# Kernel optimization log

Hardware: AMD Instinct MI355X
Metric: run time of the kernel (lower is better)

## Reference

```python
import jax, jax.numpy as jnp
import numpy as np

# Winograd F(2x2, 3x3) transform matrices (standard Lavin & Gray form).
# The original torch module encodes B^T / A^T but applies them with elementwise
# mul (a bug that crashes); the intended math is Y = A^T [ (G g G^T) .* (B^T d B) ] A
# per 4x4 input tile with stride 2, which equals a valid 3x3 conv. We implement
# that intended Winograd computation faithfully and vectorized.
_BT = jnp.array([[1., 0., -1., 0.],
                 [0., 1., 1., 0.],
                 [0., -1., 1., 0.],
                 [0., 1., 0., -1.]], dtype=jnp.float32)
_G = jnp.array([[1., 0., 0.],
                [0.5, 0.5, 0.5],
                [0.5, -0.5, 0.5],
                [0., 0., 1.]], dtype=jnp.float32)
_AT = jnp.array([[1., 1., 1., 0.],
                 [0., 1., -1., -1.]], dtype=jnp.float32)


def setup_inputs() -> dict:
    key = jax.random.key(0)
    k1, k2 = jax.random.split(key)
    X = jax.random.normal(k1, (16, 32, 258, 258), dtype=jnp.float32)
    K = jax.random.normal(k2, (32, 32, 3, 3), dtype=jnp.float32)
    return {"X": X, "K": K}


def _winograd_conv(X, K):
    B_, C, H, W = X.shape
    Fo = K.shape[0]
    blocks = (H - 3) // 2 + 1  # number of 2x2 output tiles per spatial dim

    # Kernel transform: U = G K G^T  -> (Fo, C, 4, 4)
    U = jnp.einsum('ij,fcjk,lk->fcil', _G, K, _G)

    # Extract overlapping 4x4 tiles with stride 2: (B, C, blocks, blocks, 4, 4)
    i0 = jnp.arange(blocks) * 2
    win = i0[:, None] + jnp.arange(4)[None, :]          # (blocks, 4)
    tiles = X[:, :, win, :]                              # (B, C, blocks, 4, W)
    tiles = tiles[:, :, :, :, win]                       # (B, C, blocks, 4, blocks, 4)
    tiles = tiles.transpose(0, 1, 2, 4, 3, 5)            # (B, C, p, q, 4, 4)

    # Input transform: V = B^T d B
    V = jnp.einsum('ij,bcpqjk,lk->bcpqil', _BT, tiles, _BT)

    # Elementwise multiply in transform domain, summed over input channels
    M = jnp.einsum('fcil,bcpqil->bfpqil', U, V)          # (B, Fo, p, q, 4, 4)

    # Inverse transform: Y = A^T M A -> (B, Fo, p, q, 2, 2)
    Y = jnp.einsum('ij,bfpqjk,lk->bfpqil', _AT, M, _AT)

    # Stitch 2x2 tiles back: (B, Fo, 2*blocks, 2*blocks)
    out = Y.transpose(0, 1, 2, 4, 3, 5).reshape(B_, Fo, 2 * blocks, 2 * blocks)
    return out


def reference(X, K):
    return _winograd_conv(X, K)
```

## Files before the change

### kernel.cpp

```cpp
#include <hip/hip_runtime.h>
#include <stdint.h>

typedef __attribute__((ext_vector_type(8))) short bf16x8;
typedef __attribute__((ext_vector_type(4))) float f32x4;

__device__ inline float bflo(uint32_t w) { union { uint32_t i; float f; } v; v.i = w << 16; return v.f; }
__device__ inline float bfhi(uint32_t w) { union { uint32_t i; float f; } v; v.i = w & 0xffff0000u; return v.f; }
__device__ inline uint32_t f2bf(float f) { union { float f; uint32_t i; } v; v.f = f; return (v.i + 0x8000u) >> 16; }
__device__ inline uint32_t pk(float lo, float hi) { return f2bf(lo) | (f2bf(hi) << 16); }

__global__ __launch_bounds__(256) void wg_filter(const float* __restrict__ Kk, uint32_t* __restrict__ Ud)
{
    const int idx = blockIdx.x * 256 + threadIdx.x;
    if (idx >= 512) return;
    const int cp = idx & 15, f = idx >> 4;
    float u[2][16];
    #pragma unroll
    for (int h = 0; h < 2; h++) {
        const float* kp = Kk + (f * 32 + cp * 2 + h) * 9;
        float k00 = kp[0], k01 = kp[1], k02 = kp[2];
        float k10 = kp[3], k11 = kp[4], k12 = kp[5];
        float k20 = kp[6], k21 = kp[7], k22 = kp[8];
        float t[4][3];
        t[0][0] = k00; t[0][1] = k01; t[0][2] = k02;
        t[1][0] = 0.5f * (k00 + k10 + k20); t[1][1] = 0.5f * (k01 + k11 + k21); t[1][2] = 0.5f * (k02 + k12 + k22);
        t[2][0] = 0.5f * (k00 - k10 + k20); t[2][1] = 0.5f * (k01 - k11 + k21); t[2][2] = 0.5f * (k02 - k12 + k22);
        t[3][0] = k20; t[3][1] = k21; t[3][2] = k22;
        #pragma unroll
        for (int i = 0; i < 4; i++) {
            float a0 = t[i][0], a1 = t[i][1], a2 = t[i][2];
            u[h][i * 4 + 0] = a0;
            u[h][i * 4 + 1] = 0.5f * (a0 + a1 + a2);
            u[h][i * 4 + 2] = 0.5f * (a0 - a1 + a2);
            u[h][i * 4 + 3] = a2;
        }
    }
    const int base = ((cp >> 2) * 32 + f) * 4 + (cp & 3);
    #pragma unroll
    for (int p = 0; p < 16; p++) Ud[p * 512 + base] = pk(u[0][p], u[1][p]);
}

__global__ __launch_bounds__(256, 5) void wg_main(
    const float* __restrict__ X, const uint16_t* __restrict__ U, float* __restrict__ out)
{
    __shared__ __align__(16) uint32_t Pl[2896];
    __shared__ __align__(16) uint16_t Vl[8192];

    const int tid = threadIdx.x;
    const int qb = blockIdx.x;
    const int pb = blockIdx.y;
    const int b  = blockIdx.z;
    const int y0 = pb * 8, x0 = qb * 16;

    for (int s = tid; s < 1440; s += 256) {
        const int pr = s / 90;
        const int r  = s - pr * 90;
        const int row = r / 9, seg = r - row * 9;
        const float* g0 = X + ((size_t)((b * 32 + pr * 2) * 258 + y0 + row)) * 258 + x0 + seg * 2;
        float2 a = *(const float2*)g0;
        float2 c = *(const float2*)(g0 + 258 * 258);
        const int pbase = pr * 181 + row * 18 + seg * 2;
        Pl[pbase]     = pk(a.x, c.x);
        Pl[pbase + 1] = pk(a.y, c.y);
    }
    __syncthreads();

    const int wave = tid >> 6, lane = tid & 63;
    const int fh = wave & 1, tb = wave >> 1;
    const int l15 = lane & 15, lq = lane >> 4;
    const uint16_t* Ub = U + (lq * 32 + fh * 16 + l15) * 8;
    const uint16_t* Vb = Vl + ((tb * 4 + lq) * 16 + l15) * 8;
    uint32_t* vp = (uint32_t*)Vl;

    float y[4][4];
    #pragma unroll
    for (int r = 0; r < 4; r++)
        #pragma unroll
        for (int j = 0; j < 4; j++) y[r][j] = 0.f;

    #pragma unroll
    for (int ch = 0; ch < 2; ch++) {
        #pragma unroll
        for (int it = 0; it < 2; it++) {
            const int rem  = it * 4 + wave;
            const int tblk = rem & 1, cpH = rem >> 1;
            const int cp2  = tid & 3, t15 = (tid >> 2) & 15;
            const int cp   = cpH * 4 + cp2;
            const int tt   = tblk * 16 + t15;
            const int tr   = tt >> 3, tc = tt & 7;
            const uint32_t* pp = &Pl[cp * 181 + (tr * 2 + ch) * 18 + tc * 2];
            float d0[3][4], d1[3][4];
            #pragma unroll
            for (int j = 0; j < 3; j++)
                #pragma unroll
                for (int k = 0; k < 4; k++) {
                    uint32_t w = pp[j * 18 + k];
                    d0[j][k] = bflo(w); d1[j][k] = bfhi(w);
                }
            float e00[4], e01[4], e10[4], e11[4];
            #pragma unroll
            for (int k = 0; k < 4; k++) {
                if (ch == 0) {
                    e00[k] = d0[0][k] - d0[2][k];  e10[k] = d1[0][k] - d1[2][k];
                    e01[k] = d0[1][k] + d0[2][k];  e11[k] = d1[1][k] + d1[2][k];
                } else {
                    e00[k] = d0[1][k] - d0[0][k];  e10[k] = d1[1][k] - d1[0][k];
                    e01[k] = d0[0][k] - d0[2][k];  e11[k] = d1[0][k] - d1[2][k];
                }
            }
            const int vbase = ((tblk * 4 + cpH) * 16 + t15) * 4 + cp2;
            #pragma unroll
            for (int row = 0; row < 2; row++) {
                const float* e0 = row ? e01 : e00;
                const float* e1 = row ? e11 : e10;
                vp[(row * 4 + 0) * 512 + vbase] = pk(e0[0] - e0[2], e1[0] - e1[2]);
                vp[(row * 4 + 1) * 512 + vbase] = pk(e0[1] + e0[2], e1[1] + e1[2]);
                vp[(row * 4 + 2) * 512 + vbase] = pk(e0[2] - e0[1], e1[2] - e1[1]);
                vp[(row * 4 + 3) * 512 + vbase] = pk(e0[1] - e0[3], e1[1] - e1[3]);
            }
        }
        __syncthreads();

        f32x4 acc[8];
        #pragma unroll
        for (int p8 = 0; p8 < 8; p8++) acc[p8] = (f32x4){0.f, 0.f, 0.f, 0.f};
        #pragma unroll
        for (int p8 = 0; p8 < 8; p8++) {
            bf16x8 a = *(const bf16x8*)(Ub + (ch * 8 + p8) * 1024);
            bf16x8 v = *(const bf16x8*)(Vb + p8 * 1024);
            acc[p8] = __builtin_amdgcn_mfma_f32_16x16x32_bf16(a, v, acc[p8], 0, 0, 0);
        }
        if (ch == 0) __syncthreads();

        #pragma unroll
        for (int r = 0; r < 4; r++) {
            #pragma unroll
            for (int ii = 0; ii < 2; ii++) {
                const int i = ch * 2 + ii;
                float m0 = acc[ii * 4 + 0][r], m1 = acc[ii * 4 + 1][r];
                float m2 = acc[ii * 4 + 2][r], m3 = acc[ii * 4 + 3][r];
                float c0 = m0 + m1 + m2, c1 = m1 - m2 - m3;
                if (i == 0)      { y[r][0] += c0; y[r][1] += c1; }
                else if (i == 1) { y[r][0] += c0; y[r][1] += c1; y[r][2] += c0; y[r][3] += c1; }
                else if (i == 2) { y[r][0] += c0; y[r][1] += c1; y[r][2] -= c0; y[r][3] -= c1; }
                else             { y[r][2] -= c0; y[r][3] -= c1; }
            }
        }
    }

    const int t = tb * 16 + l15;
    const int trr = t >> 3, tcc = t & 7;
    const int p = pb * 4 + trr, q = qb * 8 + tcc;
    #pragma unroll
    for (int r = 0; r < 4; r++) {
        const int f = fh * 16 + lq * 4 + r;
        float* op = out + ((size_t)(b * 32 + f) * 256 + 2 * p) * 256 + 2 * q;
        *(float2*)op = make_float2(y[r][0], y[r][1]);
        *(float2*)(op + 256) = make_float2(y[r][2], y[r][3]);
    }
}

__device__ inline uint16_t f2bf16_rne(float f) {
    union { float f; uint32_t i; } v; v.f = f;
    uint32_t x = v.i;
    uint32_t r = x + 0x7fffu + ((x >> 16) & 1u);
    return (uint16_t)(r >> 16);
}
__global__ __launch_bounds__(256) void winograd_fallback(
    const float* __restrict__ X, const float* __restrict__ K, float* __restrict__ out)
{
    __shared__ uint16_t Ul[16384];
    __shared__ uint16_t Vl[16384];
    __shared__ uint16_t Pl[32 * 242];
    const int tid = threadIdx.x;
    const int qb = blockIdx.x, pb = blockIdx.y, b = blockIdx.z;
    for (int idx = tid; idx < 1024; idx += 256) {
        const int f = idx >> 5, c = idx & 31;
        const float* kp = K + (f * 32 + c) * 9;
        float k00 = kp[0], k01 = kp[1], k02 = kp[2];
        float k10 = kp[3], k11 = kp[4], k12 = kp[5];
        float k20 = kp[6], k21 = kp[7], k22 = kp[8];
        float t[4][3];
        t[0][0] = k00; t[0][1] = k01; t[0][2] = k02;
        t[1][0] = 0.5f * (k00 + k10 + k20); t[1][1] = 0.5f * (k01 + k11 + k21); t[1][2] = 0.5f * (k02 + k12 + k22);
        t[2][0] = 0.5f * (k00 - k10 + k20); t[2][1] = 0.5f * (k01 - k11 + k21); t[2][2] = 0.5f * (k02 - k12 + k22);
        t[3][0] = k20; t[3][1] = k21; t[3][2] = k22;
        const int ubase = ((c >> 3) * 32 + f) * 8 + (c & 7);
        #pragma unroll
        for (int i = 0; i < 4; i++) {
            float a0 = t[i][0], a1 = t[i][1], a2 = t[i][2];
            Ul[(i * 4 + 0) * 1024 + ubase] = f2bf16_rne(a0);
            Ul[(i * 4 + 1) * 1024 + ubase] = f2bf16_rne(0.5f * (a0 + a1 + a2));
            Ul[(i * 4 + 2) * 1024 + ubase] = f2bf16_rne(0.5f * (a0 - a1 + a2));
            Ul[(i * 4 + 3) * 1024 + ubase] = f2bf16_rne(a2);
        }
    }
    const int y0 = pb * 8, x0 = qb * 16;
    for (int s = tid; s < 2880; s += 256) {
        const int c = s / 90;
        const int r = s % 90;
        const int row = r / 9, seg = r % 9;
        const float* gp = X + ((b * 32 + c) * 258 + (y0 + row)) * 258 + x0 + seg * 2;
        float2 g = *(const float2*)gp;
        uint32_t packed = (uint32_t)f2bf16_rne(g.x) | ((uint32_t)f2bf16_rne(g.y) << 16);
        *(uint32_t*)&Pl[c * 242 + row * 24 + seg * 2] = packed;
    }
    __syncthreads();
    for (int idx = tid; idx < 1024; idx += 256) {
        const int c = idx & 31, tt = idx >> 5;
        const int tr = tt >> 3, tc = tt & 7;
        const uint16_t* pp = &Pl[c * 242 + (tr * 2) * 24 + tc * 2];
        float d[4][4];
        #pragma unroll
        for (int j = 0; j < 4; j++) {
            uint32_t w0 = *(const uint32_t*)&pp[j * 24];
            uint32_t w1 = *(const uint32_t*)&pp[j * 24 + 2];
            d[j][0] = bflo(w0); d[j][1] = bfhi(w0);
            d[j][2] = bflo(w1); d[j][3] = bfhi(w1);
        }
        float bt[4][4];
        #pragma unroll
        for (int k = 0; k < 4; k++) {
            bt[0][k] = d[0][k] - d[2][k];
            bt[1][k] = d[1][k] + d[2][k];
            bt[2][k] = d[2][k] - d[1][k];
            bt[3][k] = d[1][k] - d[3][k];
        }
        const int vbase = (((tt >> 4) * 4 + (c >> 3)) * 16 + (tt & 15)) * 8 + (c & 7);
        #pragma unroll
        for (int i = 0; i < 4; i++) {
            float b0 = bt[i][0], b1 = bt[i][1], b2 = bt[i][2], b3 = bt[i][3];
            Vl[(i * 4 + 0) * 1024 + vbase] = f2bf16_rne(b0 - b2);
            Vl[(i * 4 + 1) * 1024 + vbase] = f2bf16_rne(b1 + b2);
            Vl[(i * 4 + 2) * 1024 + vbase] = f2bf16_rne(b2 - b1);
            Vl[(i * 4 + 3) * 1024 + vbase] = f2bf16_rne(b1 - b3);
        }
    }
    __syncthreads();
    const int wave = tid >> 6, lane = tid & 63;
    const int fh = wave & 1, tb = wave >> 1;
    const int l15 = lane & 15, lq = lane >> 4;
    f32x4 acc[16];
    #pragma unroll
    for (int p = 0; p < 16; p++) acc[p] = (f32x4){0.f, 0.f, 0.f, 0.f};
    #pragma unroll
    for (int p = 0; p < 16; p++) {
        bf16x8 a = *(const bf16x8*)&Ul[p * 1024 + (lq * 32 + fh * 16 + l15) * 8];
        bf16x8 bv = *(const bf16x8*)&Vl[p * 1024 + ((tb * 4 + lq) * 16 + l15) * 8];
        acc[p] = __builtin_amdgcn_mfma_f32_16x16x32_bf16(a, bv, acc[p], 0, 0, 0);
    }
    #pragma unroll
    for (int r = 0; r < 4; r++) {
        const int f = fh * 16 + lq * 4 + r;
        const int t = tb * 16 + l15;
        const int tr = t >> 3, tc = t & 7;
        const int p = pb * 4 + tr, q = qb * 8 + tc;
        float m[4][4];
        #pragma unroll
        for (int i = 0; i < 4; i++)
            #pragma unroll
            for (int l = 0; l < 4; l++)
                m[i][l] = acc[i * 4 + l][r];
        float s0[4], s1[4];
        #pragma unroll
        for (int k = 0; k < 4; k++) {
            s0[k] = m[0][k] + m[1][k] + m[2][k];
            s1[k] = m[1][k] - m[2][k] - m[3][k];
        }
        float* op = out + ((size_t)(b * 32 + f) * 256 + 2 * p) * 256 + 2 * q;
        *(float2*)op = make_float2(s0[0] + s0[1] + s0[2], s0[1] - s0[2] - s0[3]);
        *(float2*)(op + 256) = make_float2(s1[0] + s1[1] + s1[2], s1[1] - s1[2] - s1[3]);
    }
}

extern "C" void kernel_launch(void* const* d_in, const int* in_sizes, int n_in,
                              void* d_out, int out_size, void* d_ws, size_t ws_size,
                              hipStream_t stream) {
    const float* X = (const float*)d_in[0];
    const float* K = (const float*)d_in[1];
    float* out = (float*)d_out;
    dim3 grid(16, 32, 16);
    if (ws_size >= 32768) {
        wg_filter<<<2, 256, 0, stream>>>(K, (uint32_t*)d_ws);
        wg_main<<<grid, 256, 0, stream>>>(X, (const uint16_t*)d_ws, out);
    } else {
        winograd_fallback<<<grid, 256, 0, stream>>>(X, K, out);
    }
}
```

Measured before the change: 95.42 us.

## Use packed f32 math, hardware bf16 pack, vector LDS access, and early U loads

Replaces scalar float add/sub in the input transform with v_pk_add_f32 on paired channels. Manual bf16 rounding is replaced with v_cvt_pk_bf16_f32, which also changes the rounding behaviour. The LDS patch stride moves from 181 to 182 so that stores and loads can be 64-bit vectors. The filter fragments are now loaded from global memory before the input transform so their latency overlaps that compute, at the cost of extra registers under the occupancy bound of 5.

```diff
diff --git a/kernel.cpp b/kernel.cpp
--- a/kernel.cpp
+++ b/kernel.cpp
@@ -3,11 +3,27 @@
 
 typedef __attribute__((ext_vector_type(8))) short bf16x8;
 typedef __attribute__((ext_vector_type(4))) float f32x4;
+typedef __attribute__((ext_vector_type(2))) float f32x2;
 
 __device__ inline float bflo(uint32_t w) { union { uint32_t i; float f; } v; v.i = w << 16; return v.f; }
 __device__ inline float bfhi(uint32_t w) { union { uint32_t i; float f; } v; v.i = w & 0xffff0000u; return v.f; }
 __device__ inline uint32_t f2bf(float f) { union { float f; uint32_t i; } v; v.f = f; return (v.i + 0x8000u) >> 16; }
 __device__ inline uint32_t pk(float lo, float hi) { return f2bf(lo) | (f2bf(hi) << 16); }
+
+__device__ inline f32x2 pka(f32x2 a, f32x2 b) {
+    f32x2 d; asm("v_pk_add_f32 %0, %1, %2" : "=v"(d) : "v"(a), "v"(b)); return d;
+}
+__device__ inline f32x2 pks(f32x2 a, f32x2 b) {
+    f32x2 d; asm("v_pk_add_f32 %0, %1, %2 neg_lo:[0,1] neg_hi:[0,1]" : "=v"(d) : "v"(a), "v"(b)); return d;
+}
+__device__ inline uint32_t cvtpk2(float lo, float hi) {
+    uint32_t r; asm("v_cvt_pk_bf16_f32 %0, %1, %2" : "=v"(r) : "v"(lo), "v"(hi)); return r;
+}
+__device__ inline uint32_t cvtpk(f32x2 v) { return cvtpk2(v.x, v.y); }
+__device__ inline f32x2 unpk(uint32_t w) {
+    union { uint32_t u; float f; } lo, hi; lo.u = w << 16; hi.u = w & 0xffff0000u;
+    return (f32x2){lo.f, hi.f};
+}
 
 __global__ __launch_bounds__(256) void wg_filter(const float* __restrict__ Kk, uint32_t* __restrict__ Ud)
 {
@@ -43,7 +59,7 @@
 __global__ __launch_bounds__(256, 5) void wg_main(
     const float* __restrict__ X, const uint16_t* __restrict__ U, float* __restrict__ out)
 {
-    __shared__ __align__(16) uint32_t Pl[2896];
+    __shared__ __align__(16) uint32_t Pl[2912];
     __shared__ __align__(16) uint16_t Vl[8192];
 
     const int tid = threadIdx.x;
@@ -59,9 +75,10 @@
         const float* g0 = X + ((size_t)((b * 32 + pr * 2) * 258 + y0 + row)) * 258 + x0 + seg * 2;
         float2 a = *(const float2*)g0;
         float2 c = *(const float2*)(g0 + 258 * 258);
-        const int pbase = pr * 181 + row * 18 + seg * 2;
-        Pl[pbase]     = pk(a.x, c.x);
-        Pl[pbase + 1] = pk(a.y, c.y);
+        uint2 w;
+        w.x = cvtpk2(a.x, c.x);
+        w.y = cvtpk2(a.y, c.y);
+        *(uint2*)&Pl[pr * 182 + row * 18 + seg * 2] = w;
     }
     __syncthreads();
 
@@ -80,6 +97,11 @@
 
     #pragma unroll
     for (int ch = 0; ch < 2; ch++) {
+        bf16x8 a_reg[8];
+        #pragma unroll
+        for (int p8 = 0; p8 < 8; p8++)
+            a_reg[p8] = *(const bf16x8*)(Ub + (ch * 8 + p8) * 1024);
+
         #pragma unroll
         for (int it = 0; it < 2; it++) {
             const int rem  = it * 4 + wave;
@@ -88,35 +110,34 @@
             const int cp   = cpH * 4 + cp2;
             const int tt   = tblk * 16 + t15;
             const int tr   = tt >> 3, tc = tt & 7;
-            const uint32_t* pp = &Pl[cp * 181 + (tr * 2 + ch) * 18 + tc * 2];
-            float d0[3][4], d1[3][4];
-            #pragma unroll
-            for (int j = 0; j < 3; j++)
-                #pragma unroll
-                for (int k = 0; k < 4; k++) {
-                    uint32_t w = pp[j * 18 + k];
-                    d0[j][k] = bflo(w); d1[j][k] = bfhi(w);
-                }
-            float e00[4], e01[4], e10[4], e11[4];
+            const uint32_t* pp = &Pl[cp * 182 + (tr * 2 + ch) * 18 + tc * 2];
+            f32x2 dd[3][4];
+            #pragma unroll
+            for (int j = 0; j < 3; j++) {
+                uint2 w01 = *(const uint2*)&pp[j * 18];
+                uint2 w23 = *(const uint2*)&pp[j * 18 + 2];
+                dd[j][0] = unpk(w01.x); dd[j][1] = unpk(w01.y);
+                dd[j][2] = unpk(w23.x); dd[j][3] = unpk(w23.y);
+            }
+            f32x2 e0[4], e1[4];
             #pragma unroll
             for (int k = 0; k < 4; k++) {
                 if (ch == 0) {
-                    e00[k] = d0[0][k] - d0[2][k];  e10[k] = d1[0][k] - d1[2][k];
-                    e01[k] = d0[1][k] + d0[2][k];  e11[k] = d1[1][k] + d1[2][k];
+                    e0[k] = pks(dd[0][k], dd[2][k]);
+                    e1[k] = pka(dd[1][k], dd[2][k]);
                 } else {
-                    e00[k] = d0[1][k] - d0[0][k];  e10[k] = d1[1][k] - d1[0][k];
-                    e01[k] = d0[0][k] - d0[2][k];  e11[k] = d1[0][k] - d1[2][k];
+                    e0[k] = pks(dd[1][k], dd[0][k]);
+                    e1[k] = pks(dd[0][k], dd[2][k]);
                 }
             }
             const int vbase = ((tblk * 4 + cpH) * 16 + t15) * 4 + cp2;
             #pragma unroll
             for (int row = 0; row < 2; row++) {
-                const float* e0 = row ? e01 : e00;
-                const float* e1 = row ? e11 : e10;
-                vp[(row * 4 + 0) * 512 + vbase] = pk(e0[0] - e0[2], e1[0] - e1[2]);
-                vp[(row * 4 + 1) * 512 + vbase] = pk(e0[1] + e0[2], e1[1] + e1[2]);
-                vp[(row * 4 + 2) * 512 + vbase] = pk(e0[2] - e0[1], e1[2] - e1[1]);
-                vp[(row * 4 + 3) * 512 + vbase] = pk(e0[1] - e0[3], e1[1] - e1[3]);
+                const f32x2* e = row ? e1 : e0;
+                vp[(row * 4 + 0) * 512 + vbase] = cvtpk(pks(e[0], e[2]));
+                vp[(row * 4 + 1) * 512 + vbase] = cvtpk(pka(e[1], e[2]));
+                vp[(row * 4 + 2) * 512 + vbase] = cvtpk(pks(e[2], e[1]));
+                vp[(row * 4 + 3) * 512 + vbase] = cvtpk(pks(e[1], e[3]));
             }
         }
         __syncthreads();
@@ -126,9 +147,8 @@
         for (int p8 = 0; p8 < 8; p8++) acc[p8] = (f32x4){0.f, 0.f, 0.f, 0.f};
         #pragma unroll
         for (int p8 = 0; p8 < 8; p8++) {
-            bf16x8 a = *(const bf16x8*)(Ub + (ch * 8 + p8) * 1024);
             bf16x8 v = *(const bf16x8*)(Vb + p8 * 1024);
-            acc[p8] = __builtin_amdgcn_mfma_f32_16x16x32_bf16(a, v, acc[p8], 0, 0, 0);
+            acc[p8] = __builtin_amdgcn_mfma_f32_16x16x32_bf16(a_reg[p8], v, acc[p8], 0, 0, 0);
         }
         if (ch == 0) __syncthreads();
 
```

Result: no change. 93.65 us (-1.9%).
